# Optimization experiments

Measured on AMD Instinct MI355X. Metric: run time of the kernel, lower is better.

Reference implementation:

```python
import jax, jax.numpy as jnp
import numpy as np

B, N, D = 2, 2048, 1024
CTX, TV = 256, 250
H, DH = 16, 64
INNER = H * DH          # 1024
FF = 4 * D              # 4096 (GEGLU inner)
SCALE = DH ** -0.5


def _layernorm(x, g, b):
    mu = x.mean(-1, keepdims=True)
    var = ((x - mu) ** 2).mean(-1, keepdims=True)
    return (x - mu) / jnp.sqrt(var + 1e-5) * g + b


def _attn(xq, ctx, wq, wk, wv, wo, bo):
    b, n, _ = xq.shape
    m = ctx.shape[1]
    q = (xq @ wq).reshape(b, n, H, DH)
    k = (ctx @ wk).reshape(b, m, H, DH)
    v = (ctx @ wv).reshape(b, m, H, DH)
    sim = jnp.einsum('bihd,bjhd->bhij', q, k) * SCALE
    att = jax.nn.softmax(sim, axis=-1)
    out = jnp.einsum('bhij,bjhd->bihd', att, v).reshape(b, n, INNER)
    return out @ wo + bo


def _sin_pe(T, d):
    pos = jnp.arange(T, dtype=jnp.float32)[:, None]
    den = jnp.power(10000.0, 2.0 * jnp.arange(d // 2, dtype=jnp.float32) / d)
    ang = pos / den                                  # [T, d/2]
    return jnp.stack([jnp.sin(ang), jnp.cos(ang)], -1).reshape(T, d)


def setup_inputs() -> dict:
    key = jax.random.key(0)
    ks = jax.random.split(key, 40)
    w = lambda k, s: jax.random.normal(k, s, jnp.float32) * 0.02
    inp = {
        'x': jax.random.normal(ks[0], (B, N, D), jnp.float32),
        'context': jax.random.normal(ks[1], (B, CTX, D), jnp.float32),
        'hint_control': jax.random.normal(ks[2], (B, TV, D), jnp.float32),
        'ln1_g': jnp.ones((D,)), 'ln1_b': jnp.zeros((D,)),
        'ln2_g': jnp.ones((D,)), 'ln2_b': jnp.zeros((D,)),
        'ln3_g': jnp.ones((D,)), 'ln3_b': jnp.zeros((D,)),
        'ln4_g': jnp.ones((D,)), 'ln4_b': jnp.zeros((D,)),
        'a1_wq': w(ks[3], (D, INNER)), 'a1_wk': w(ks[4], (D, INNER)),
        'a1_wv': w(ks[5], (D, INNER)), 'a1_wo': w(ks[6], (INNER, D)),
        'a1_bo': jnp.zeros((D,)),
        'a2_wq': w(ks[7], (D, INNER)), 'a2_wk': w(ks[8], (D, INNER)),
        'a2_wv': w(ks[9], (D, INNER)), 'a2_wo': w(ks[10], (INNER, D)),
        'a2_bo': jnp.zeros((D,)),
        'a3_wq': w(ks[11], (D, INNER)), 'a3_wk': w(ks[12], (D, INNER)),
        'a3_wv': w(ks[13], (D, INNER)), 'a3_wo': w(ks[14], (INNER, D)),
        'a3_bo': jnp.zeros((D,)),
        'ff_w1': w(ks[15], (D, 2 * FF)), 'ff_b1': jnp.zeros((2 * FF,)),
        'ff_w2': w(ks[16], (FF, D)), 'ff_b2': jnp.zeros((D,)),
    }
    return inp


def reference(x, context, hint_control,
              ln1_g, ln1_b, ln2_g, ln2_b, ln3_g, ln3_b, ln4_g, ln4_b,
              a1_wq, a1_wk, a1_wv, a1_wo, a1_bo,
              a2_wq, a2_wk, a2_wv, a2_wo, a2_bo,
              a3_wq, a3_wk, a3_wv, a3_wo, a3_bo,
              ff_w1, ff_b1, ff_w2, ff_b2):
    # attn1: self-attention (disable_self_attn=False -> context is x itself)
    h = _layernorm(x, ln1_g, ln1_b)
    x = _attn(h, h, a1_wq, a1_wk, a1_wv, a1_wo, a1_bo) + x
    # attn2: cross-attention over context
    h = _layernorm(x, ln2_g, ln2_b)
    x = _attn(h, context, a2_wq, a2_wk, a2_wv, a2_wo, a2_bo) + x
    # attn3: video cross-attention with sinusoidal PE added to hint_control
    hint = hint_control + _sin_pe(hint_control.shape[1], D)[None]
    h = _layernorm(x, ln4_g, ln4_b)
    x = _attn(h, hint, a3_wq, a3_wk, a3_wv, a3_wo, a3_bo) + x
    # GEGLU feed-forward
    h = _layernorm(x, ln3_g, ln3_b)
    proj = h @ ff_w1 + ff_b1
    a, gate = jnp.split(proj, 2, axis=-1)
    x = (a * jax.nn.gelu(gate, approximate=False)) @ ff_w2 + ff_b2 + x
    return x
```

## Files before the change

kernel.cpp:

```cpp
#include <hip/hip_runtime.h>
#include <cstdint>

typedef unsigned short u16;
typedef __bf16 bf16x8 __attribute__((ext_vector_type(8)));
typedef float f32x4 __attribute__((ext_vector_type(4)));

__device__ __forceinline__ u16 f2bf(float f) {
  union { float f; uint32_t u; } x; x.f = f;
  uint32_t r = x.u + 0x7FFFu + ((x.u >> 16) & 1u);
  return (u16)(r >> 16);
}
__device__ __forceinline__ bf16x8 ld8s(const u16* p) {
  return *reinterpret_cast<const bf16x8*>(p);
}
__device__ __forceinline__ float geluf(float x) {
  return 0.5f * x * (1.f + erff(x * 0.70710678118654752f));
}
__device__ __forceinline__ uint32_t cvtpk(float a, float b) {
  uint32_t r;
  asm("v_cvt_pk_bf16_f32 %0, %1, %2" : "=v"(r) : "v"(a), "v"(b));
  return r;
}
__device__ __forceinline__ void gload16(const u16* g, u16* l) {
  __builtin_amdgcn_global_load_lds(
      (__attribute__((address_space(1))) void*)const_cast<u16*>(g),
      (__attribute__((address_space(3))) void*)l, 16, 0, 0);
}

struct PrepJob {
  const void* src; void* dst;
  int K, N, mode, row_off, ldo, s_lo, s_hi, blk0;
};
struct PrepArgs { PrepJob j[17]; };

__global__ __launch_bounds__(256) void wprep_kernel(PrepArgs a) {
  __shared__ float tile[32][33];
  int bid = blockIdx.x;
  int t = threadIdx.x;
  const float* src = nullptr; void* dst = nullptr;
  int K = 0, N = 0, mode = 0, roff = 0, ldo = 0, slo = 0, shi = 0, bl = 0;
#pragma unroll
  for (int i = 0; i < 17; ++i) {
    int lo = a.j[i].blk0;
    int hi = (i == 16) ? 0x7fffffff : a.j[i + 1].blk0;
    if (bid >= lo && bid < hi) {
      src = (const float*)a.j[i].src; dst = a.j[i].dst;
      K = a.j[i].K; N = a.j[i].N; mode = a.j[i].mode; roff = a.j[i].row_off;
      ldo = a.j[i].ldo; slo = a.j[i].s_lo; shi = a.j[i].s_hi; bl = bid - lo;
    }
  }
  (void)K;
  if (mode <= 1) {
    int nb = N >> 5;
    int bx = bl % nb, by = bl / nb;
    int tx = t & 31, ty = t >> 5;
    int n = bx * 32 + tx, kbase = by * 32;
#pragma unroll
    for (int r = 0; r < 4; ++r)
      tile[ty + r * 8][tx] = src[(size_t)(kbase + ty + r * 8) * N + n];
    __syncthreads();
#pragma unroll
    for (int r = 0; r < 4; ++r) {
      int nl = ty + r * 8, ng = bx * 32 + nl;
      int orow;
      if (mode == 0) orow = roff + ng;
      else {
        if (ng < 4096) orow = ((ng >> 4) << 5) + (ng & 15);
        else { int t2 = ng - 4096; orow = ((t2 >> 4) << 5) + 16 + (t2 & 15); }
      }
      float v = tile[tx][nl];
      if (mode == 0 && orow >= slo && orow < shi) v *= 0.18033688011112042f;
      ((u16*)dst)[(size_t)orow * ldo + kbase + tx] = f2bf(v);
    }
  } else if (mode == 2) {
    int idx = bl * 1024 + t * 4;
    float4 v = *reinterpret_cast<const float4*>(src + idx);
    ushort4 o;
    o.x = f2bf(v.x); o.y = f2bf(v.y); o.z = f2bf(v.z); o.w = f2bf(v.w);
    *reinterpret_cast<ushort4*>((u16*)dst + idx) = o;
  } else if (mode == 3) {
    int row = bl;
    int tt = row % 250;
    int d0 = t * 4;
    int i0 = d0 >> 1;
    float den0 = powf(10000.f, (float)i0 / 512.f);
    float den1 = powf(10000.f, (float)(i0 + 1) / 512.f);
    float a0 = (float)tt / den0, a1 = (float)tt / den1;
    const float* hp = src + (size_t)row * 1024 + d0;
    u16* op = (u16*)dst + (size_t)row * 1024 + d0;
    op[0] = f2bf(hp[0] + sinf(a0));
    op[1] = f2bf(hp[1] + cosf(a0));
    op[2] = f2bf(hp[2] + sinf(a1));
    op[3] = f2bf(hp[3] + cosf(a1));
  } else {
    int i2 = bl * 256 + t;
    int g = i2 >> 5, s2 = i2 & 31;
    int c2 = (s2 < 16) ? (g * 16 + s2) : (4096 + g * 16 + (s2 - 16));
    ((float*)dst)[i2] = src[c2];
  }
}

__global__ __launch_bounds__(256) void ln_kernel(const float* __restrict__ x,
                                                 const float* __restrict__ g,
                                                 const float* __restrict__ b,
                                                 u16* __restrict__ out) {
  int row = blockIdx.x;
  int tid = threadIdx.x;
  int l = tid & 63, w = tid >> 6;
  const float4 v = reinterpret_cast<const float4*>(x + (size_t)row * 1024)[tid];
  float s = v.x + v.y + v.z + v.w;
#pragma unroll
  for (int d = 1; d < 64; d <<= 1) s += __shfl_xor(s, d, 64);
  __shared__ float red[8];
  if (l == 0) red[w] = s;
  __syncthreads();
  float mean = (red[0] + red[1] + red[2] + red[3]) * (1.f / 1024.f);
  float dx = v.x - mean, dy = v.y - mean, dz = v.z - mean, dw = v.w - mean;
  float vs = dx * dx + dy * dy + dz * dz + dw * dw;
#pragma unroll
  for (int d = 1; d < 64; d <<= 1) vs += __shfl_xor(vs, d, 64);
  if (l == 0) red[4 + w] = vs;
  __syncthreads();
  float var = (red[4] + red[5] + red[6] + red[7]) * (1.f / 1024.f);
  float rstd = rsqrtf(var + 1e-5f);
  const float4 g4 = reinterpret_cast<const float4*>(g)[tid];
  const float4 b4 = reinterpret_cast<const float4*>(b)[tid];
  ushort4 o;
  o.x = f2bf(dx * rstd * g4.x + b4.x);
  o.y = f2bf(dy * rstd * g4.y + b4.y);
  o.z = f2bf(dz * rstd * g4.z + b4.z);
  o.w = f2bf(dw * rstd * g4.w + b4.w);
  reinterpret_cast<ushort4*>(out + (size_t)row * 1024)[tid] = o;
}

template <int EPI>
__global__ __launch_bounds__(512, 2) void gemm256_kernel(
    const u16* __restrict__ A, int lda, const u16* __restrict__ Bt,
    void* __restrict__ Cv, int ldc, const float* __restrict__ bias,
    int M, int N, int K) {
  __shared__ __align__(16) u16 As[2][256 * 64];
  __shared__ __align__(16) u16 Bs[2][256 * 64];
  int t = threadIdx.x;
  int l = t & 63, w = t >> 6;
  int wm = w >> 2, wn = w & 3;
  int lr = l & 15, lg = l >> 4;
  int gx = gridDim.x;
  int nwg = gx * gridDim.y;
  int orig = blockIdx.y * gx + blockIdx.x;
  int qq = nwg >> 3, rr = nwg & 7;
  int xcd = orig & 7, lin = orig >> 3;
  int wg = (xcd < rr ? xcd * (qq + 1) : rr * (qq + 1) + (xcd - rr) * qq) + lin;
  int bx = wg % gx, by = wg / gx;
  int row0 = by * 256, n0 = bx * 256;

  int lrow8 = l >> 3, lchunk = l & 7;
  int csrc = (lchunk ^ lrow8) * 8;
  int keyA = lr & 7;

  f32x4 acc[8][4];
#pragma unroll
  for (int i = 0; i < 8; ++i)
#pragma unroll
    for (int j = 0; j < 4; ++j) acc[i][j] = f32x4{0.f, 0.f, 0.f, 0.f};

  auto stage = [&](int buf, int k0) {
#pragma unroll
    for (int q = 0; q < 4; ++q) {
      int rbase = w * 32 + q * 8;
      int r = rbase + lrow8;
      gload16(&A[(size_t)(row0 + r) * lda + k0 + csrc], &As[buf][rbase * 64]);
      gload16(&Bt[(size_t)(n0 + r) * K + k0 + csrc], &Bs[buf][rbase * 64]);
    }
  };

  int nk = K >> 6;
  stage(0, 0);
  __syncthreads();
  int cur = 0;
  for (int ti = 0; ti < nk; ++ti) {
    if (ti + 1 < nk) stage(cur ^ 1, (ti + 1) << 6);
#pragma unroll
    for (int kk = 0; kk < 2; ++kk) {
      int chunk = (((kk << 2) + lg) ^ keyA) << 3;
      bf16x8 af[8];
#pragma unroll
      for (int mi = 0; mi < 8; ++mi)
        af[mi] = ld8s(&As[cur][(wm * 128 + mi * 16 + lr) * 64 + chunk]);
      bf16x8 bfv[4];
#pragma unroll
      for (int ni = 0; ni < 4; ++ni)
        bfv[ni] = ld8s(&Bs[cur][(wn * 64 + ni * 16 + lr) * 64 + chunk]);
#pragma unroll
      for (int mi = 0; mi < 8; ++mi)
#pragma unroll
        for (int ni = 0; ni < 4; ++ni)
          acc[mi][ni] = __builtin_amdgcn_mfma_f32_16x16x32_bf16(af[mi], bfv[ni], acc[mi][ni], 0, 0, 0);
    }
    __syncthreads();
    cur ^= 1;
  }

#pragma unroll
  for (int mi = 0; mi < 8; ++mi) {
    int rowb = row0 + wm * 128 + mi * 16 + lg * 4;
    if (EPI == 2) {
#pragma unroll
      for (int p = 0; p < 2; ++p) {
        int colA = n0 + wn * 64 + p * 32 + lr;
        int colG = colA + 16;
        int ocol = ((n0 + wn * 64) >> 1) + p * 16 + lr;
#pragma unroll
        for (int r = 0; r < 4; ++r) {
          float av = acc[mi][2 * p][r] + bias[colA];
          float gv = acc[mi][2 * p + 1][r] + bias[colG];
          ((u16*)Cv)[(size_t)(rowb + r) * ldc + ocol] = f2bf(av * geluf(gv));
        }
      }
    } else {
#pragma unroll
      for (int ni = 0; ni < 4; ++ni) {
        int gcol = n0 + wn * 64 + ni * 16 + lr;
#pragma unroll
        for (int r = 0; r < 4; ++r)
          ((u16*)Cv)[(size_t)(rowb + r) * ldc + gcol] = f2bf(acc[mi][ni][r]);
      }
    }
  }
}

template <int EPI, bool GUARD>
__global__ __launch_bounds__(256) void gemm_bt_kernel(
    const u16* __restrict__ A, int lda, const u16* __restrict__ Bt,
    void* __restrict__ Cv, int ldc, const float* __restrict__ bias,
    const float* __restrict__ res, int M, int N, int K) {
  __shared__ __align__(16) u16 As[128 * 64];
  __shared__ __align__(16) u16 Bs[128 * 64];
  int t = threadIdx.x;
  int l = t & 63, w = t >> 6;
  int wm = w >> 1, wn = w & 1;
  int lr = l & 15, lg = l >> 4;
  int gx = gridDim.x;
  int nwg = gx * gridDim.y;
  int orig = blockIdx.y * gx + blockIdx.x;
  int qq = nwg >> 3, rr = nwg & 7;
  int xcd = orig & 7, lin = orig >> 3;
  int wg = (xcd < rr ? xcd * (qq + 1) : rr * (qq + 1) + (xcd - rr) * qq) + lin;
  int bx = wg % gx, by = wg / gx;
  int row0 = by * 128, n0 = bx * 128;

  int lrow8 = l >> 3, lchunk = l & 7;
  f32x4 acc[4][4];
#pragma unroll
  for (int i = 0; i < 4; ++i)
#pragma unroll
    for (int j = 0; j < 4; ++j) acc[i][j] = f32x4{0.f, 0.f, 0.f, 0.f};

  int keyA = lr & 7;
  for (int k0 = 0; k0 < K; k0 += 64) {
#pragma unroll
    for (int q = 0; q < 4; ++q) {
      int rbase = w * 32 + q * 8;
      int r = rbase + lrow8;
      int csrc = (lchunk ^ lrow8) * 8;
      int ga = row0 + r;
      if (GUARD) { if (ga > M - 1) ga = M - 1; }
      gload16(&A[(size_t)ga * lda + k0 + csrc], &As[rbase * 64]);
      int gb = n0 + r;
      gload16(&Bt[(size_t)gb * K + k0 + csrc], &Bs[rbase * 64]);
    }
    __syncthreads();
#pragma unroll
    for (int kk = 0; kk < 2; ++kk) {
      bf16x8 af[4], bfv[4];
#pragma unroll
      for (int mi = 0; mi < 4; ++mi)
        af[mi] = ld8s(&As[(wm * 64 + mi * 16 + lr) * 64 + ((((kk << 2) + lg) ^ keyA) << 3)]);
#pragma unroll
      for (int ni = 0; ni < 4; ++ni)
        bfv[ni] = ld8s(&Bs[(wn * 64 + ni * 16 + lr) * 64 + ((((kk << 2) + lg) ^ keyA) << 3)]);
#pragma unroll
      for (int mi = 0; mi < 4; ++mi)
#pragma unroll
        for (int ni = 0; ni < 4; ++ni)
          acc[mi][ni] = __builtin_amdgcn_mfma_f32_16x16x32_bf16(af[mi], bfv[ni], acc[mi][ni], 0, 0, 0);
    }
    __syncthreads();
  }

#pragma unroll
  for (int mi = 0; mi < 4; ++mi) {
    int rowb = row0 + wm * 64 + mi * 16 + lg * 4;
    if (EPI == 2) {
#pragma unroll
      for (int p = 0; p < 2; ++p) {
        int colA = n0 + wn * 64 + p * 32 + lr;
        int colG = colA + 16;
        int ocol = ((n0 + wn * 64) >> 1) + p * 16 + lr;
#pragma unroll
        for (int r = 0; r < 4; ++r) {
          int grow = rowb + r;
          float av = acc[mi][2 * p][r] + bias[colA];
          float gv = acc[mi][2 * p + 1][r] + bias[colG];
          ((u16*)Cv)[(size_t)grow * ldc + ocol] = f2bf(av * geluf(gv));
        }
      }
    } else {
#pragma unroll
      for (int ni = 0; ni < 4; ++ni) {
        int gcol = n0 + wn * 64 + ni * 16 + lr;
#pragma unroll
        for (int r = 0; r < 4; ++r) {
          int grow = rowb + r;
          if (GUARD && grow >= M) continue;
          float v = acc[mi][ni][r];
          if (EPI == 0)
            ((u16*)Cv)[(size_t)grow * ldc + gcol] = f2bf(v);
          else
            ((float*)Cv)[(size_t)grow * ldc + gcol] =
                v + bias[gcol] + res[(size_t)grow * ldc + gcol];
        }
      }
    }
  }
}

template <bool TG>
__global__ __launch_bounds__(256) void attn_kernel(
    const u16* __restrict__ Q, int qs, int qoff,
    const u16* __restrict__ KV, int kvs, int koff, int voff,
    int m, u16* __restrict__ O) {
  int b = blockIdx.z, h = blockIdx.y;
  int t = threadIdx.x;
  int l = t & 63, w = t >> 6;
  int lr = l & 15, lg = l >> 4;
  int q0 = blockIdx.x * 128 + w * 16;
  __shared__ __align__(16) u16 Ks[2][64 * 64];
  __shared__ __align__(16) u16 Vt[2][64 * 64];
  __shared__ __align__(16) u16 Pl[4][16 * 64];

  const u16* qrowA = Q + (size_t)((b << 11) + q0 + lr) * qs + qoff + h * 64;
  const u16* qrowB = qrowA + (size_t)64 * qs;
  bf16x8 qa0 = ld8s(qrowA + lg * 8), qa1 = ld8s(qrowA + 32 + lg * 8);
  bf16x8 qb0 = ld8s(qrowB + lg * 8), qb1 = ld8s(qrowB + 32 + lg * 8);

  f32x4 oA[4], oB[4];
  float psA = 0.f, psB = 0.f;
#pragma unroll
  for (int r = 0; r < 4; ++r) { oA[r] = f32x4{0.f, 0.f, 0.f, 0.f}; oB[r] = f32x4{0.f, 0.f, 0.f, 0.f}; }

  const u16* kvb = KV + (size_t)b * m * kvs + h * 64;
  int kj = t >> 3, kc = t & 7;
  int srcsw = ((l & 7) ^ (l >> 3)) << 3;
  int psw = (lr & 7) ^ ((lr & 8) >> 1);

  {
#pragma unroll
    for (int q2 = 0; q2 < 2; ++q2) {
      int gr = w * 16 + q2 * 8 + (l >> 3);
      if (TG) { if (gr > m - 1) gr = m - 1; }
      gload16(kvb + (size_t)gr * kvs + koff + srcsw, &Ks[0][(w * 16 + q2 * 8) * 64]);
    }
    int jv = kj * 2;
    int gv0 = jv, gv1 = jv + 1;
    if (TG) { if (gv0 > m - 1) gv0 = m - 1; if (gv1 > m - 1) gv1 = m - 1; }
    uint4 va = *reinterpret_cast<const uint4*>(kvb + (size_t)gv0 * kvs + voff + kc * 8);
    uint4 vb2 = *reinterpret_cast<const uint4*>(kvb + (size_t)gv1 * kvs + voff + kc * 8);
    const u16* vap = reinterpret_cast<const u16*>(&va);
    const u16* vbp = reinterpret_cast<const u16*>(&vb2);
    int jb = jv >> 3, jlow = jv & 7;
#pragma unroll
    for (int i = 0; i < 8; ++i) {
      int d = kc * 8 + i;
      int key = (d ^ (d >> 3)) & 7;
      uint32_t pk = (uint32_t)vap[i] | ((uint32_t)vbp[i] << 16);
      *reinterpret_cast<uint32_t*>(&Vt[0][d * 64 + ((jb ^ key) << 3) + jlow]) = pk;
    }
  }
  __syncthreads();

  int nj = (m + 63) >> 6;
  int cur = 0;
  for (int jt = 0; jt < nj; ++jt) {
    int j0 = jt << 6;
    bool hn = (jt + 1 < nj);
    uint4 va, vb2;
    if (hn) {
      int j0n = j0 + 64;
#pragma unroll
      for (int q2 = 0; q2 < 2; ++q2) {
        int gr = j0n + w * 16 + q2 * 8 + (l >> 3);
        if (TG) { if (gr > m - 1) gr = m - 1; }
        gload16(kvb + (size_t)gr * kvs + koff + srcsw, &Ks[cur ^ 1][(w * 16 + q2 * 8) * 64]);
      }
      int jv = kj * 2;
      int gv0 = j0n + jv, gv1 = j0n + jv + 1;
      if (TG) { if (gv0 > m - 1) gv0 = m - 1; if (gv1 > m - 1) gv1 = m - 1; }
      va = *reinterpret_cast<const uint4*>(kvb + (size_t)gv0 * kvs + voff + kc * 8);
      vb2 = *reinterpret_cast<const uint4*>(kvb + (size_t)gv1 * kvs + voff + kc * 8);
    }

    const u16* Kb = Ks[cur];
    f32x4 sA[4], sB[4];
#pragma unroll
    for (int c = 0; c < 4; ++c) {
      sA[c] = f32x4{0.f, 0.f, 0.f, 0.f};
      sB[c] = f32x4{0.f, 0.f, 0.f, 0.f};
      bf16x8 k0 = ld8s(&Kb[(c * 16 + lr) * 64 + ((lg ^ (lr & 7)) << 3)]);
      bf16x8 k1 = ld8s(&Kb[(c * 16 + lr) * 64 + (((4 + lg) ^ (lr & 7)) << 3)]);
      sA[c] = __builtin_amdgcn_mfma_f32_16x16x32_bf16(k0, qa0, sA[c], 0, 0, 0);
      sA[c] = __builtin_amdgcn_mfma_f32_16x16x32_bf16(k1, qa1, sA[c], 0, 0, 0);
      sB[c] = __builtin_amdgcn_mfma_f32_16x16x32_bf16(k0, qb0, sB[c], 0, 0, 0);
      sB[c] = __builtin_amdgcn_mfma_f32_16x16x32_bf16(k1, qb1, sB[c], 0, 0, 0);
    }

    if (hn) {
      const u16* vap = reinterpret_cast<const u16*>(&va);
      const u16* vbp = reinterpret_cast<const u16*>(&vb2);
      int jv = kj * 2;
      int jb = jv >> 3, jlow = jv & 7;
#pragma unroll
      for (int i = 0; i < 8; ++i) {
        int d = kc * 8 + i;
        int key = (d ^ (d >> 3)) & 7;
        uint32_t pk = (uint32_t)vap[i] | ((uint32_t)vbp[i] << 16);
        *reinterpret_cast<uint32_t*>(&Vt[cur ^ 1][d * 64 + ((jb ^ key) << 3) + jlow]) = pk;
      }
    }

    bool tail = TG && (j0 + 64 > m);
    const u16* Vb = Vt[cur];
    bf16x8 vfr[2][4];

    {
      uint32_t pk[8];
#pragma unroll
      for (int c = 0; c < 4; ++c) {
        float p[4];
#pragma unroll
        for (int r = 0; r < 4; ++r) {
          float v = exp2f(sA[c][r]);
          if (tail && (j0 + c * 16 + lg * 4 + r >= m)) v = 0.f;
          p[r] = v; psA += v;
        }
        pk[2 * c] = cvtpk(p[0], p[1]);
        pk[2 * c + 1] = cvtpk(p[2], p[3]);
      }
#pragma unroll
      for (int c = 0; c < 4; ++c) {
        int phys = (2 * c + (lg >> 1)) ^ psw;
        uint2 u; u.x = pk[2 * c]; u.y = pk[2 * c + 1];
        *reinterpret_cast<uint2*>(&Pl[w][lr * 64 + (phys << 3) + ((lg & 1) << 2)]) = u;
      }
#pragma unroll
      for (int ks = 0; ks < 2; ++ks) {
        int physp = (ks * 4 + lg) ^ psw;
        bf16x8 pb = ld8s(&Pl[w][lr * 64 + (physp << 3)]);
#pragma unroll
        for (int dt = 0; dt < 4; ++dt) {
          int d = dt * 16 + lr;
          int key = (d ^ (d >> 3)) & 7;
          vfr[ks][dt] = ld8s(&Vb[d * 64 + ((((ks << 2) + lg) ^ key) << 3)]);
          oA[dt] = __builtin_amdgcn_mfma_f32_16x16x32_bf16(vfr[ks][dt], pb, oA[dt], 0, 0, 0);
        }
      }
    }
    {
      uint32_t pk[8];
#pragma unroll
      for (int c = 0; c < 4; ++c) {
        float p[4];
#pragma unroll
        for (int r = 0; r < 4; ++r) {
          float v = exp2f(sB[c][r]);
          if (tail && (j0 + c * 16 + lg * 4 + r >= m)) v = 0.f;
          p[r] = v; psB += v;
        }
        pk[2 * c] = cvtpk(p[0], p[1]);
        pk[2 * c + 1] = cvtpk(p[2], p[3]);
      }
#pragma unroll
      for (int c = 0; c < 4; ++c) {
        int phys = (2 * c + (lg >> 1)) ^ psw;
        uint2 u; u.x = pk[2 * c]; u.y = pk[2 * c + 1];
        *reinterpret_cast<uint2*>(&Pl[w][lr * 64 + (phys << 3) + ((lg & 1) << 2)]) = u;
      }
#pragma unroll
      for (int ks = 0; ks < 2; ++ks) {
        int physp = (ks * 4 + lg) ^ psw;
        bf16x8 pb = ld8s(&Pl[w][lr * 64 + (physp << 3)]);
#pragma unroll
        for (int dt = 0; dt < 4; ++dt)
          oB[dt] = __builtin_amdgcn_mfma_f32_16x16x32_bf16(vfr[ks][dt], pb, oB[dt], 0, 0, 0);
      }
    }
    __syncthreads();
    cur ^= 1;
  }

  psA += __shfl_xor(psA, 16, 64); psA += __shfl_xor(psA, 32, 64);
  psB += __shfl_xor(psB, 16, 64); psB += __shfl_xor(psB, 32, 64);
  float invA = 1.f / psA, invB = 1.f / psB;
  {
    int grow = (b << 11) + q0 + lr;
    u16* op = O + (size_t)grow * 1024 + h * 64 + lg * 4;
#pragma unroll
    for (int dt = 0; dt < 4; ++dt) {
      uint2 u;
      u.x = cvtpk(oA[dt][0] * invA, oA[dt][1] * invA);
      u.y = cvtpk(oA[dt][2] * invA, oA[dt][3] * invA);
      *reinterpret_cast<uint2*>(op + dt * 16) = u;
    }
    u16* op2 = op + (size_t)64 * 1024;
#pragma unroll
    for (int dt = 0; dt < 4; ++dt) {
      uint2 u;
      u.x = cvtpk(oB[dt][0] * invB, oB[dt][1] * invB);
      u.y = cvtpk(oB[dt][2] * invB, oB[dt][3] * invB);
      *reinterpret_cast<uint2*>(op2 + dt * 16) = u;
    }
  }
}

extern "C" void kernel_launch(void* const* d_in, const int* in_sizes, int n_in,
                              void* d_out, int out_size, void* d_ws, size_t ws_size,
                              hipStream_t stream) {
  const float* x_in = (const float*)d_in[0];
  const float* ctx_in = (const float*)d_in[1];
  const float* hint_in = (const float*)d_in[2];
  const float* ln1g = (const float*)d_in[3]; const float* ln1b = (const float*)d_in[4];
  const float* ln2g = (const float*)d_in[5]; const float* ln2b = (const float*)d_in[6];
  const float* ln3g = (const float*)d_in[7]; const float* ln3b = (const float*)d_in[8];
  const float* ln4g = (const float*)d_in[9]; const float* ln4b = (const float*)d_in[10];
  const float* a1wq = (const float*)d_in[11]; const float* a1wk = (const float*)d_in[12];
  const float* a1wv = (const float*)d_in[13]; const float* a1wo = (const float*)d_in[14];
  const float* a1bo = (const float*)d_in[15];
  const float* a2wq = (const float*)d_in[16]; const float* a2wk = (const float*)d_in[17];
  const float* a2wv = (const float*)d_in[18]; const float* a2wo = (const float*)d_in[19];
  const float* a2bo = (const float*)d_in[20];
  const float* a3wq = (const float*)d_in[21]; const float* a3wk = (const float*)d_in[22];
  const float* a3wv = (const float*)d_in[23]; const float* a3wo = (const float*)d_in[24];
  const float* a3bo = (const float*)d_in[25];
  const float* ffw1 = (const float*)d_in[26]; const float* ffb1 = (const float*)d_in[27];
  const float* ffw2 = (const float*)d_in[28]; const float* ffb2 = (const float*)d_in[29];

  char* wsb = (char*)d_ws;
  size_t off = 0;
  auto alloc = [&](size_t bytes) -> void* {
    void* p = wsb + off;
    off += (bytes + 255) & ~(size_t)255;
    return p;
  };
  u16* wqkv1t = (u16*)alloc(3072ull * 1024 * 2);
  u16* wo1t = (u16*)alloc(1024ull * 1024 * 2);
  u16* wq2t = (u16*)alloc(1024ull * 1024 * 2);
  u16* wkv2t = (u16*)alloc(2048ull * 1024 * 2);
  u16* wo2t = (u16*)alloc(1024ull * 1024 * 2);
  u16* wq3t = (u16*)alloc(1024ull * 1024 * 2);
  u16* wkv3t = (u16*)alloc(2048ull * 1024 * 2);
  u16* wo3t = (u16*)alloc(1024ull * 1024 * 2);
  u16* w1t = (u16*)alloc(8192ull * 1024 * 2);
  u16* w2t = (u16*)alloc(1024ull * 4096 * 2);
  float* b1p = (float*)alloc(8192ull * 4);
  u16* hintbf = (u16*)alloc(500ull * 1024 * 2);
  u16* ctxbf = (u16*)alloc(512ull * 1024 * 2);
  float* xbuf = (float*)alloc(4096ull * 1024 * 4);
  u16* hbf = (u16*)alloc(4096ull * 1024 * 2);
  u16* attnout = (u16*)alloc(4096ull * 1024 * 2);
  u16* qbuf = (u16*)alloc(4096ull * 1024 * 2);
  u16* kvbuf = (u16*)alloc(512ull * 2048 * 2);
  u16* qkv = (u16*)alloc(4096ull * 4096 * 2);
  u16* gbuf = qkv;

  PrepArgs pa;
  int bi = 0, bc = 0;
  auto addJ = [&](const void* s, void* d, int K, int N, int mode, int roff,
                  int ldo, int slo, int shi, int nblk) {
    pa.j[bi].src = s; pa.j[bi].dst = d; pa.j[bi].K = K; pa.j[bi].N = N;
    pa.j[bi].mode = mode; pa.j[bi].row_off = roff; pa.j[bi].ldo = ldo;
    pa.j[bi].s_lo = slo; pa.j[bi].s_hi = shi; pa.j[bi].blk0 = bc;
    bc += nblk; ++bi;
  };
  addJ(a1wq, wqkv1t, 1024, 1024, 0, 0, 1024, 0, 1024, 1024);
  addJ(a1wk, wqkv1t, 1024, 1024, 0, 1024, 1024, 0, 0, 1024);
  addJ(a1wv, wqkv1t, 1024, 1024, 0, 2048, 1024, 0, 0, 1024);
  addJ(a1wo, wo1t, 1024, 1024, 0, 0, 1024, 0, 0, 1024);
  addJ(a2wq, wq2t, 1024, 1024, 0, 0, 1024, 0, 1024, 1024);
  addJ(a2wk, wkv2t, 1024, 1024, 0, 0, 1024, 0, 0, 1024);
  addJ(a2wv, wkv2t, 1024, 1024, 0, 1024, 1024, 0, 0, 1024);
  addJ(a2wo, wo2t, 1024, 1024, 0, 0, 1024, 0, 0, 1024);
  addJ(a3wq, wq3t, 1024, 1024, 0, 0, 1024, 0, 1024, 1024);
  addJ(a3wk, wkv3t, 1024, 1024, 0, 0, 1024, 0, 0, 1024);
  addJ(a3wv, wkv3t, 1024, 1024, 0, 1024, 1024, 0, 0, 1024);
  addJ(a3wo, wo3t, 1024, 1024, 0, 0, 1024, 0, 0, 1024);
  addJ(ffw1, w1t, 1024, 8192, 1, 0, 1024, 0, 0, 8192);
  addJ(ffw2, w2t, 4096, 1024, 0, 0, 4096, 0, 0, 4096);
  addJ(ctx_in, ctxbf, 0, 0, 2, 0, 0, 0, 0, 512);
  addJ(hint_in, hintbf, 0, 0, 3, 0, 0, 0, 0, 500);
  addJ(ffb1, b1p, 0, 0, 4, 0, 0, 0, 0, 32);
  wprep_kernel<<<bc, 256, 0, stream>>>(pa);

  ln_kernel<<<4096, 256, 0, stream>>>(x_in, ln1g, ln1b, hbf);
  gemm256_kernel<0><<<dim3(12, 16), 512, 0, stream>>>(hbf, 1024, wqkv1t, qkv, 3072,
                                                      nullptr, 4096, 3072, 1024);
  attn_kernel<false><<<dim3(16, 16, 2), 256, 0, stream>>>(qkv, 3072, 0, qkv, 3072, 1024, 2048,
                                                          2048, attnout);
  gemm_bt_kernel<1, false><<<dim3(8, 32), 256, 0, stream>>>(attnout, 1024, wo1t, xbuf, 1024,
                                                            a1bo, x_in, 4096, 1024, 1024);

  ln_kernel<<<4096, 256, 0, stream>>>(xbuf, ln2g, ln2b, hbf);
  gemm_bt_kernel<0, false><<<dim3(8, 32), 256, 0, stream>>>(hbf, 1024, wq2t, qbuf, 1024,
                                                            nullptr, nullptr, 4096, 1024, 1024);
  gemm_bt_kernel<0, false><<<dim3(16, 4), 256, 0, stream>>>(ctxbf, 1024, wkv2t, kvbuf, 2048,
                                                            nullptr, nullptr, 512, 2048, 1024);
  attn_kernel<false><<<dim3(16, 16, 2), 256, 0, stream>>>(qbuf, 1024, 0, kvbuf, 2048, 0, 1024,
                                                          256, attnout);
  gemm_bt_kernel<1, false><<<dim3(8, 32), 256, 0, stream>>>(attnout, 1024, wo2t, xbuf, 1024,
                                                            a2bo, xbuf, 4096, 1024, 1024);

  ln_kernel<<<4096, 256, 0, stream>>>(xbuf, ln4g, ln4b, hbf);
  gemm_bt_kernel<0, false><<<dim3(8, 32), 256, 0, stream>>>(hbf, 1024, wq3t, qbuf, 1024,
                                                            nullptr, nullptr, 4096, 1024, 1024);
  gemm_bt_kernel<0, true><<<dim3(16, 4), 256, 0, stream>>>(hintbf, 1024, wkv3t, kvbuf, 2048,
                                                           nullptr, nullptr, 500, 2048, 1024);
  attn_kernel<true><<<dim3(16, 16, 2), 256, 0, stream>>>(qbuf, 1024, 0, kvbuf, 2048, 0, 1024,
                                                         250, attnout);
  gemm_bt_kernel<1, false><<<dim3(8, 32), 256, 0, stream>>>(attnout, 1024, wo3t, xbuf, 1024,
                                                            a3bo, xbuf, 4096, 1024, 1024);

  ln_kernel<<<4096, 256, 0, stream>>>(xbuf, ln3g, ln3b, hbf);
  gemm256_kernel<2><<<dim3(32, 16), 512, 0, stream>>>(hbf, 1024, w1t, gbuf, 4096,
                                                      b1p, 4096, 8192, 1024);
  gemm_bt_kernel<1, false><<<dim3(8, 32), 256, 0, stream>>>(gbuf, 4096, w2t, d_out, 1024,
                                                            ffb2, xbuf, 4096, 1024, 4096);
}
```

Before: 532.9 us.

## Prefetch two K-tiles ahead with explicit vmcnt waits in GEMM kernels

Both GEMM kernels now keep two LDS tile buffers in flight. Tile ti+2 is issued after compute on tile ti, and s_waitcnt vmcnt(8) waits only for the older tile's loads. The aim is to hide global-to-LDS latency behind MFMA work instead of stalling on a full drain each iteration. It also raises wave priority during the MFMA section. The smaller kernel doubles its LDS use, which may lower occupancy, and the hand-written vmcnt counts depend on each stage issuing exactly 8 loads per thread.

```diff
diff --git a/kernel.cpp b/kernel.cpp
--- a/kernel.cpp
+++ b/kernel.cpp
@@ -175,10 +175,17 @@
 
   int nk = K >> 6;
   stage(0, 0);
-  __syncthreads();
+  if (nk > 1) {
+    stage(1, 64);
+    asm volatile("s_waitcnt vmcnt(8)" ::: "memory");
+  } else {
+    asm volatile("s_waitcnt vmcnt(0)" ::: "memory");
+  }
+  __builtin_amdgcn_sched_barrier(0);
+  __builtin_amdgcn_s_barrier();
   int cur = 0;
   for (int ti = 0; ti < nk; ++ti) {
-    if (ti + 1 < nk) stage(cur ^ 1, (ti + 1) << 6);
+    __builtin_amdgcn_s_setprio(1);
 #pragma unroll
     for (int kk = 0; kk < 2; ++kk) {
       int chunk = (((kk << 2) + lg) ^ keyA) << 3;
@@ -196,7 +203,17 @@
         for (int ni = 0; ni < 4; ++ni)
           acc[mi][ni] = __builtin_amdgcn_mfma_f32_16x16x32_bf16(af[mi], bfv[ni], acc[mi][ni], 0, 0, 0);
     }
-    __syncthreads();
+    __builtin_amdgcn_s_setprio(0);
+    __builtin_amdgcn_sched_barrier(0);
+    __builtin_amdgcn_s_barrier();
+    if (ti + 2 < nk) {
+      stage(cur, (ti + 2) << 6);
+      asm volatile("s_waitcnt vmcnt(8)" ::: "memory");
+    } else {
+      asm volatile("s_waitcnt vmcnt(0)" ::: "memory");
+    }
+    __builtin_amdgcn_sched_barrier(0);
+    __builtin_amdgcn_s_barrier();
     cur ^= 1;
   }
 
@@ -233,8 +250,8 @@
     const u16* __restrict__ A, int lda, const u16* __restrict__ Bt,
     void* __restrict__ Cv, int ldc, const float* __restrict__ bias,
     const float* __restrict__ res, int M, int N, int K) {
-  __shared__ __align__(16) u16 As[128 * 64];
-  __shared__ __align__(16) u16 Bs[128 * 64];
+  __shared__ __align__(16) u16 As[2][128 * 64];
+  __shared__ __align__(16) u16 Bs[2][128 * 64];
   int t = threadIdx.x;
   int l = t & 63, w = t >> 6;
   int wm = w >> 1, wn = w & 1;
@@ -249,42 +266,66 @@
   int row0 = by * 128, n0 = bx * 128;
 
   int lrow8 = l >> 3, lchunk = l & 7;
+  int csrc = (lchunk ^ lrow8) * 8;
+  int keyA = lr & 7;
   f32x4 acc[4][4];
 #pragma unroll
   for (int i = 0; i < 4; ++i)
 #pragma unroll
     for (int j = 0; j < 4; ++j) acc[i][j] = f32x4{0.f, 0.f, 0.f, 0.f};
 
-  int keyA = lr & 7;
-  for (int k0 = 0; k0 < K; k0 += 64) {
+  auto stage = [&](int buf, int k0) {
 #pragma unroll
     for (int q = 0; q < 4; ++q) {
       int rbase = w * 32 + q * 8;
       int r = rbase + lrow8;
-      int csrc = (lchunk ^ lrow8) * 8;
       int ga = row0 + r;
       if (GUARD) { if (ga > M - 1) ga = M - 1; }
-      gload16(&A[(size_t)ga * lda + k0 + csrc], &As[rbase * 64]);
-      int gb = n0 + r;
-      gload16(&Bt[(size_t)gb * K + k0 + csrc], &Bs[rbase * 64]);
-    }
-    __syncthreads();
+      gload16(&A[(size_t)ga * lda + k0 + csrc], &As[buf][rbase * 64]);
+      gload16(&Bt[(size_t)(n0 + r) * K + k0 + csrc], &Bs[buf][rbase * 64]);
+    }
+  };
+
+  int nk = K >> 6;
+  stage(0, 0);
+  if (nk > 1) {
+    stage(1, 64);
+    asm volatile("s_waitcnt vmcnt(8)" ::: "memory");
+  } else {
+    asm volatile("s_waitcnt vmcnt(0)" ::: "memory");
+  }
+  __builtin_amdgcn_sched_barrier(0);
+  __builtin_amdgcn_s_barrier();
+  int cur = 0;
+  for (int ti = 0; ti < nk; ++ti) {
+    __builtin_amdgcn_s_setprio(1);
 #pragma unroll
     for (int kk = 0; kk < 2; ++kk) {
       bf16x8 af[4], bfv[4];
 #pragma unroll
       for (int mi = 0; mi < 4; ++mi)
-        af[mi] = ld8s(&As[(wm * 64 + mi * 16 + lr) * 64 + ((((kk << 2) + lg) ^ keyA) << 3)]);
+        af[mi] = ld8s(&As[cur][(wm * 64 + mi * 16 + lr) * 64 + ((((kk << 2) + lg) ^ keyA) << 3)]);
 #pragma unroll
       for (int ni = 0; ni < 4; ++ni)
-        bfv[ni] = ld8s(&Bs[(wn * 64 + ni * 16 + lr) * 64 + ((((kk << 2) + lg) ^ keyA) << 3)]);
+        bfv[ni] = ld8s(&Bs[cur][(wn * 64 + ni * 16 + lr) * 64 + ((((kk << 2) + lg) ^ keyA) << 3)]);
 #pragma unroll
       for (int mi = 0; mi < 4; ++mi)
 #pragma unroll
         for (int ni = 0; ni < 4; ++ni)
           acc[mi][ni] = __builtin_amdgcn_mfma_f32_16x16x32_bf16(af[mi], bfv[ni], acc[mi][ni], 0, 0, 0);
     }
-    __syncthreads();
+    __builtin_amdgcn_s_setprio(0);
+    __builtin_amdgcn_sched_barrier(0);
+    __builtin_amdgcn_s_barrier();
+    if (ti + 2 < nk) {
+      stage(cur, (ti + 2) << 6);
+      asm volatile("s_waitcnt vmcnt(8)" ::: "memory");
+    } else {
+      asm volatile("s_waitcnt vmcnt(0)" ::: "memory");
+    }
+    __builtin_amdgcn_sched_barrier(0);
+    __builtin_amdgcn_s_barrier();
+    cur ^= 1;
   }
 
 #pragma unroll
```

Result: faster. 508.1 us (-4.6%).
